# Optimization experiments

Hardware: AMD Instinct MI355X
Metric: run time of the kernel (lower is better)

## Reference

```python
import jax, jax.numpy as jnp
import numpy as np

NX, NY, D, K = 20000, 50000, 64, 8
NUM_BATCHES = 2


def _knn_np(px, py, bx, by, k):
    # Batched exact kNN via chunked squared-distance + argpartition (mirrors torch_cluster.knn under no_grad).
    pp = (px * px).sum(1)
    idx = np.empty((py.shape[0], k), np.int32)
    chunk = 4096
    for s in range(0, py.shape[0], chunk):
        q = py[s:s + chunk]
        d = (q * q).sum(1)[:, None] + pp[None, :] - 2.0 * (q @ px.T)
        d = np.where(by[s:s + chunk, None] == bx[None, :], d, np.inf)
        idx[s:s + chunk] = np.argpartition(d, k, axis=1)[:, :k].astype(np.int32)
    return idx


def setup_inputs() -> dict:
    rng = np.random.default_rng(0)
    pos_x = (rng.random((NX, 3)) * 10.0).astype(np.float32)
    pos_y = (rng.random((NY, 3)) * 10.0).astype(np.float32)
    bx = np.repeat(np.arange(NUM_BATCHES), NX // NUM_BATCHES).astype(np.int32)
    by = np.repeat(np.arange(NUM_BATCHES), NY // NUM_BATCHES).astype(np.int32)
    x_idx = _knn_np(pos_x, pos_y, bx, by, K).reshape(-1)            # [NY*K]
    y_idx = np.repeat(np.arange(NY, dtype=np.int32), K)             # [NY*K]

    key = jax.random.key(0)
    ks = jax.random.split(key, 6)

    def lin(k, fi, fo):
        return jax.random.normal(k, (fi, fo), jnp.float32) / np.sqrt(fi).astype(np.float32)

    return {
        "x": jax.random.normal(ks[0], (NX, D), jnp.float32),
        "pos_x": jnp.asarray(pos_x),
        "pos_y": jnp.asarray(pos_y),
        "x_idx": jnp.asarray(x_idx),
        "y_idx": jnp.asarray(y_idx),
        # ResnetBlockFC 1: size_in=D+3, size_h=D, size_out=D (shortcut linear, no bias)
        "W0a": lin(ks[1], D + 3, D), "b0a": jnp.zeros((D,), jnp.float32),
        "W1a": lin(ks[2], D, D),     "b1a": jnp.zeros((D,), jnp.float32),
        "Wsa": lin(ks[3], D + 3, D),
        # ResnetBlockFC 2: size_in=size_h=size_out=D (identity shortcut)
        "W0b": lin(ks[4], D, D),     "b0b": jnp.zeros((D,), jnp.float32),
        "W1b": lin(ks[5], D, D),     "b1b": jnp.zeros((D,), jnp.float32),
    }


def reference(x, pos_x, pos_y, x_idx, y_idx, W0a, b0a, W1a, b1a, Wsa, W0b, b0b, W1b, b1b):
    # gather + positional diff (diff computed under no_grad in the original)
    diff = jax.lax.stop_gradient(pos_x[x_idx] - pos_y[y_idx])        # [E, 3]
    h = jnp.concatenate([x[x_idx], diff], axis=1)                    # [E, D+3]
    # ResnetBlockFC 1: out = shortcut(h) + fc1(relu(fc0(relu(h))))
    net = jax.nn.relu(h) @ W0a + b0a
    dx = jax.nn.relu(net) @ W1a + b1a
    h = h @ Wsa + dx                                                 # [E, D]
    # ResnetBlockFC 2 (identity shortcut)
    net = jax.nn.relu(h) @ W0b + b0b
    h = h + jax.nn.relu(net) @ W1b + b1b                             # [E, D]
    # scatter-max back to query points (every query has exactly K edges)
    out = jax.ops.segment_max(h, y_idx, num_segments=NY)             # [NY, D]
    return out
```

## Files before the change

kernel.cpp:

```cpp
#include <hip/hip_runtime.h>


typedef _Float16 f16x8 __attribute__((ext_vector_type(8)));
typedef float    f32x4 __attribute__((ext_vector_type(4)));

constexpr int NROWS   = 50000 * 8;
constexpr int NTILES  = NROWS / 16;
constexpr int NFRAG   = 48;
constexpr int TSTRIDE = 72;
constexpr int BW      = 8;

__global__ __launch_bounds__(512, 4)
void pointnet_fused(const float* __restrict__ x,
                    const float* __restrict__ pos_x,
                    const float* __restrict__ pos_y,
                    const int*   __restrict__ x_idx,
                    const float* __restrict__ W0a, const float* __restrict__ b0a,
                    const float* __restrict__ W1a, const float* __restrict__ b1a,
                    const float* __restrict__ Wsa,
                    const float* __restrict__ W0b, const float* __restrict__ b0b,
                    const float* __restrict__ W1b, const float* __restrict__ b1b,
                    float* __restrict__ out)
{
    __shared__ __align__(16) _Float16 bfrag[NFRAG * 64 * 8];
    __shared__ __align__(16) _Float16 trans[BW][16 * TSTRIDE];

    const int tid = threadIdx.x;

    for (int p = tid; p < NFRAG * 64; p += 512) {
        const int f = p >> 6;
        const int l = p & 63;
        const float* W; int krows, fl;
        if (f < 12)      { W = W0a; krows = 67; fl = f; }
        else if (f < 20) { W = W1a; krows = 64; fl = f - 12; }
        else if (f < 32) { W = Wsa; krows = 67; fl = f - 20; }
        else if (f < 40) { W = W0b; krows = 64; fl = f - 32; }
        else             { W = W1b; krows = 64; fl = f - 40; }
        const int s = fl >> 2, t = fl & 3;
        const int n = t * 16 + (l & 15);
        const int kbase = s * 32 + (l >> 4) * 8;
        f16x8 v;
#pragma unroll
        for (int j = 0; j < 8; ++j) {
            const int k = kbase + j;
            v[j] = (_Float16)((k < krows) ? W[k * 64 + n] : 0.0f);
        }
        *(f16x8*)&bfrag[p * 8] = v;
    }
    __syncthreads();

    const int lane = tid & 63;
    const int wv   = tid >> 6;
    const int n0   = lane & 15;
    const int q    = lane >> 4;

    float bias0a[4], bias1a[4], bias0b[4], bias1b[4];
#pragma unroll
    for (int t = 0; t < 4; ++t) {
        bias0a[t] = b0a[t * 16 + n0];
        bias1a[t] = b1a[t * 16 + n0];
        bias0b[t] = b0b[t * 16 + n0];
        bias1b[t] = b1b[t * 16 + n0];
    }

    _Float16* tbuf = trans[wv];
    const int gwave  = blockIdx.x * BW + wv;
    const int nwaves = gridDim.x * BW;

    for (int tile = gwave; tile < NTILES; tile += nwaves) {
        const int row = tile * 16 + n0;
        const int xi  = x_idx[row];
        const float* xp = x + (long)xi * 64;
        f16x8 hn[3], hr[3];
#pragma unroll
        for (int s = 0; s < 2; ++s) {
            const float4* src = (const float4*)(xp + s * 32 + q * 8);
            float4 v0 = src[0], v1 = src[1];
            float vals[8] = {v0.x, v0.y, v0.z, v0.w, v1.x, v1.y, v1.z, v1.w};
#pragma unroll
            for (int j = 0; j < 8; ++j) {
                const float fv = vals[j];
                hn[s][j] = (_Float16)fv;
                hr[s][j] = (_Float16)(fv > 0.0f ? fv : 0.0f);
            }
        }
        {
            f16x8 z = {};
            hn[2] = z; hr[2] = z;
            if (q == 0) {
                const int yi = row >> 3;
#pragma unroll
                for (int j = 0; j < 3; ++j) {
                    const float d = pos_x[xi * 3 + j] - pos_y[yi * 3 + j];
                    hn[2][j] = (_Float16)d;
                    hr[2][j] = (_Float16)(d > 0.0f ? d : 0.0f);
                }
            }
        }

        f32x4 acc[4];
#pragma unroll
        for (int t = 0; t < 4; ++t)
            acc[t] = (f32x4){bias0a[t], bias0a[t], bias0a[t], bias0a[t]};
#pragma unroll
        for (int s = 0; s < 3; ++s)
#pragma unroll
            for (int t = 0; t < 4; ++t) {
                f16x8 b = *(const f16x8*)&bfrag[((s * 4 + t) * 64 + lane) * 8];
                acc[t] = __builtin_amdgcn_mfma_f32_16x16x32_f16(hr[s], b, acc[t], 0, 0, 0);
            }

        __threadfence_block();
#pragma unroll
        for (int t = 0; t < 4; ++t)
#pragma unroll
            for (int r = 0; r < 4; ++r) {
                float v = acc[t][r];
                tbuf[(q * 4 + r) * TSTRIDE + t * 16 + n0] = (_Float16)(v > 0.0f ? v : 0.0f);
            }
        __threadfence_block();
        f16x8 a2[2];
#pragma unroll
        for (int s = 0; s < 2; ++s)
            a2[s] = *(const f16x8*)&tbuf[n0 * TSTRIDE + s * 32 + q * 8];

        f32x4 acc2[4];
#pragma unroll
        for (int t = 0; t < 4; ++t)
            acc2[t] = (f32x4){bias1a[t], bias1a[t], bias1a[t], bias1a[t]};
#pragma unroll
        for (int s = 0; s < 2; ++s)
#pragma unroll
            for (int t = 0; t < 4; ++t) {
                f16x8 b = *(const f16x8*)&bfrag[((12 + s * 4 + t) * 64 + lane) * 8];
                acc2[t] = __builtin_amdgcn_mfma_f32_16x16x32_f16(a2[s], b, acc2[t], 0, 0, 0);
            }
#pragma unroll
        for (int s = 0; s < 3; ++s)
#pragma unroll
            for (int t = 0; t < 4; ++t) {
                f16x8 b = *(const f16x8*)&bfrag[((20 + s * 4 + t) * 64 + lane) * 8];
                acc2[t] = __builtin_amdgcn_mfma_f32_16x16x32_f16(hn[s], b, acc2[t], 0, 0, 0);
            }

        __threadfence_block();
#pragma unroll
        for (int t = 0; t < 4; ++t)
#pragma unroll
            for (int r = 0; r < 4; ++r) {
                float v = acc2[t][r];
                tbuf[(q * 4 + r) * TSTRIDE + t * 16 + n0] = (_Float16)(v > 0.0f ? v : 0.0f);
            }
        __threadfence_block();
        f16x8 a4[2];
#pragma unroll
        for (int s = 0; s < 2; ++s)
            a4[s] = *(const f16x8*)&tbuf[n0 * TSTRIDE + s * 32 + q * 8];

        f32x4 acc3[4];
#pragma unroll
        for (int t = 0; t < 4; ++t)
            acc3[t] = (f32x4){bias0b[t], bias0b[t], bias0b[t], bias0b[t]};
#pragma unroll
        for (int s = 0; s < 2; ++s)
#pragma unroll
            for (int t = 0; t < 4; ++t) {
                f16x8 b = *(const f16x8*)&bfrag[((32 + s * 4 + t) * 64 + lane) * 8];
                acc3[t] = __builtin_amdgcn_mfma_f32_16x16x32_f16(a4[s], b, acc3[t], 0, 0, 0);
            }

        __threadfence_block();
#pragma unroll
        for (int t = 0; t < 4; ++t)
#pragma unroll
            for (int r = 0; r < 4; ++r) {
                float v = acc3[t][r];
                tbuf[(q * 4 + r) * TSTRIDE + t * 16 + n0] = (_Float16)(v > 0.0f ? v : 0.0f);
            }
        __threadfence_block();
        f16x8 a5[2];
#pragma unroll
        for (int s = 0; s < 2; ++s)
            a5[s] = *(const f16x8*)&tbuf[n0 * TSTRIDE + s * 32 + q * 8];

        f32x4 acc4[4];
#pragma unroll
        for (int t = 0; t < 4; ++t) {
            acc4[t] = acc2[t];
            acc4[t][0] += bias1b[t]; acc4[t][1] += bias1b[t];
            acc4[t][2] += bias1b[t]; acc4[t][3] += bias1b[t];
        }
#pragma unroll
        for (int s = 0; s < 2; ++s)
#pragma unroll
            for (int t = 0; t < 4; ++t) {
                f16x8 b = *(const f16x8*)&bfrag[((40 + s * 4 + t) * 64 + lane) * 8];
                acc4[t] = __builtin_amdgcn_mfma_f32_16x16x32_f16(a5[s], b, acc4[t], 0, 0, 0);
            }

#pragma unroll
        for (int t = 0; t < 4; ++t) {
            float pm = fmaxf(fmaxf(acc4[t][0], acc4[t][1]),
                             fmaxf(acc4[t][2], acc4[t][3]));
            pm = fmaxf(pm, __shfl_xor(pm, 16, 64));
            if ((q & 1) == 0) {
                const int y = tile * 2 + (q >> 1);
                out[(long)y * 64 + t * 16 + n0] = pm;
            }
        }
    }
}

extern "C" void kernel_launch(void* const* d_in, const int* in_sizes, int n_in,
                              void* d_out, int out_size, void* d_ws, size_t ws_size,
                              hipStream_t stream) {
    (void)in_sizes; (void)n_in; (void)d_ws; (void)ws_size; (void)out_size;
    pointnet_fused<<<512, 512, 0, stream>>>(
        (const float*)d_in[0],
        (const float*)d_in[1],
        (const float*)d_in[2],
        (const int*)  d_in[3],
        (const float*)d_in[5],  (const float*)d_in[6],
        (const float*)d_in[7],  (const float*)d_in[8],
        (const float*)d_in[9],
        (const float*)d_in[10], (const float*)d_in[11],
        (const float*)d_in[12], (const float*)d_in[13],
        (float*)d_out);
}
```

Measured before the change: 126.6 us.

## Process two 16-row tiles per wave with interleaved MFMAs and atomic work queue

Each wave now handles a pair of 16-row tiles at once, interleaving the two tiles' MFMA chains so independent matrix ops can hide each other's latency, and sharing each B-fragment LDS load across both tiles. Static grid-stride tile assignment is replaced by a global atomic counter (reset with a memset in the workspace) that hands out tile pairs dynamically for load balancing. This raises register pressure, which could cut occupancy or cause spills under the 512x4 launch bound, and adds one atomic per pair plus a memset launch.

```diff
diff --git a/kernel.cpp b/kernel.cpp
--- a/kernel.cpp
+++ b/kernel.cpp
@@ -5,10 +5,36 @@
 typedef float    f32x4 __attribute__((ext_vector_type(4)));
 
 constexpr int NROWS   = 50000 * 8;
-constexpr int NTILES  = NROWS / 16;
+constexpr int NPAIRS  = NROWS / 32;
 constexpr int NFRAG   = 48;
 constexpr int TSTRIDE = 72;
 constexpr int BW      = 8;
+
+static __device__ __forceinline__ f16x8 relu8(f16x8 v) {
+    f16x8 r;
+#pragma unroll
+    for (int j = 0; j < 8; ++j) {
+        _Float16 x = v[j];
+        r[j] = x > (_Float16)0 ? x : (_Float16)0;
+    }
+    return r;
+}
+
+static __device__ __forceinline__ void xpose_relu(const f32x4* acc, _Float16* tbuf,
+                                                  int q, int n0, f16x8* af) {
+    __threadfence_block();
+#pragma unroll
+    for (int t = 0; t < 4; ++t)
+#pragma unroll
+        for (int r = 0; r < 4; ++r) {
+            float v = acc[t][r];
+            tbuf[(q * 4 + r) * TSTRIDE + t * 16 + n0] = (_Float16)(v > 0.0f ? v : 0.0f);
+        }
+    __threadfence_block();
+#pragma unroll
+    for (int s = 0; s < 2; ++s)
+        af[s] = *(const f16x8*)&tbuf[n0 * TSTRIDE + s * 32 + q * 8];
+}
 
 __global__ __launch_bounds__(512, 4)
 void pointnet_fused(const float* __restrict__ x,
@@ -20,7 +46,8 @@
                     const float* __restrict__ Wsa,
                     const float* __restrict__ W0b, const float* __restrict__ b0b,
                     const float* __restrict__ W1b, const float* __restrict__ b1b,
-                    float* __restrict__ out)
+                    float* __restrict__ out,
+                    int* __restrict__ ctr)
 {
     __shared__ __align__(16) _Float16 bfrag[NFRAG * 64 * 8];
     __shared__ __align__(16) _Float16 trans[BW][16 * TSTRIDE];
@@ -64,157 +91,148 @@
     }
 
     _Float16* tbuf = trans[wv];
-    const int gwave  = blockIdx.x * BW + wv;
-    const int nwaves = gridDim.x * BW;
-
-    for (int tile = gwave; tile < NTILES; tile += nwaves) {
-        const int row = tile * 16 + n0;
-        const int xi  = x_idx[row];
-        const float* xp = x + (long)xi * 64;
-        f16x8 hn[3], hr[3];
-#pragma unroll
-        for (int s = 0; s < 2; ++s) {
-            const float4* src = (const float4*)(xp + s * 32 + q * 8);
-            float4 v0 = src[0], v1 = src[1];
-            float vals[8] = {v0.x, v0.y, v0.z, v0.w, v1.x, v1.y, v1.z, v1.w};
-#pragma unroll
-            for (int j = 0; j < 8; ++j) {
-                const float fv = vals[j];
-                hn[s][j] = (_Float16)fv;
-                hr[s][j] = (_Float16)(fv > 0.0f ? fv : 0.0f);
-            }
-        }
-        {
+
+    for (;;) {
+        int pr = 0;
+        if (lane == 0) pr = atomicAdd(ctr, 1);
+        pr = __shfl(pr, 0, 64);
+        if (pr >= NPAIRS) break;
+
+        f16x8 hn[2][3];
+#pragma unroll
+        for (int u = 0; u < 2; ++u) {
+            const int row = pr * 32 + u * 16 + n0;
+            const int xi  = x_idx[row];
+            const float* xp = x + (long)xi * 64;
+#pragma unroll
+            for (int s = 0; s < 2; ++s) {
+                const float4* src = (const float4*)(xp + s * 32 + q * 8);
+                float4 v0 = src[0], v1 = src[1];
+                float vals[8] = {v0.x, v0.y, v0.z, v0.w, v1.x, v1.y, v1.z, v1.w};
+#pragma unroll
+                for (int j = 0; j < 8; ++j)
+                    hn[u][s][j] = (_Float16)vals[j];
+            }
             f16x8 z = {};
-            hn[2] = z; hr[2] = z;
+            hn[u][2] = z;
             if (q == 0) {
                 const int yi = row >> 3;
 #pragma unroll
-                for (int j = 0; j < 3; ++j) {
-                    const float d = pos_x[xi * 3 + j] - pos_y[yi * 3 + j];
-                    hn[2][j] = (_Float16)d;
-                    hr[2][j] = (_Float16)(d > 0.0f ? d : 0.0f);
+                for (int j = 0; j < 3; ++j)
+                    hn[u][2][j] = (_Float16)(pos_x[xi * 3 + j] - pos_y[yi * 3 + j]);
+            }
+        }
+
+        f16x8 hr[2][3];
+#pragma unroll
+        for (int u = 0; u < 2; ++u)
+#pragma unroll
+            for (int s = 0; s < 3; ++s)
+                hr[u][s] = relu8(hn[u][s]);
+
+        f32x4 A1[2][4];
+#pragma unroll
+        for (int u = 0; u < 2; ++u)
+#pragma unroll
+            for (int t = 0; t < 4; ++t)
+                A1[u][t] = (f32x4){bias0a[t], bias0a[t], bias0a[t], bias0a[t]};
+#pragma unroll
+        for (int s = 0; s < 3; ++s)
+#pragma unroll
+            for (int t = 0; t < 4; ++t) {
+                f16x8 b = *(const f16x8*)&bfrag[((s * 4 + t) * 64 + lane) * 8];
+                A1[0][t] = __builtin_amdgcn_mfma_f32_16x16x32_f16(hr[0][s], b, A1[0][t], 0, 0, 0);
+                A1[1][t] = __builtin_amdgcn_mfma_f32_16x16x32_f16(hr[1][s], b, A1[1][t], 0, 0, 0);
+            }
+
+        f16x8 a2[2][2];
+        xpose_relu(A1[0], tbuf, q, n0, a2[0]);
+        xpose_relu(A1[1], tbuf, q, n0, a2[1]);
+
+        f32x4 A2[2][4];
+#pragma unroll
+        for (int u = 0; u < 2; ++u)
+#pragma unroll
+            for (int t = 0; t < 4; ++t)
+                A2[u][t] = (f32x4){bias1a[t], bias1a[t], bias1a[t], bias1a[t]};
+#pragma unroll
+        for (int s = 0; s < 2; ++s)
+#pragma unroll
+            for (int t = 0; t < 4; ++t) {
+                f16x8 b = *(const f16x8*)&bfrag[((12 + s * 4 + t) * 64 + lane) * 8];
+                A2[0][t] = __builtin_amdgcn_mfma_f32_16x16x32_f16(a2[0][s], b, A2[0][t], 0, 0, 0);
+                A2[1][t] = __builtin_amdgcn_mfma_f32_16x16x32_f16(a2[1][s], b, A2[1][t], 0, 0, 0);
+            }
+#pragma unroll
+        for (int s = 0; s < 3; ++s)
+#pragma unroll
+            for (int t = 0; t < 4; ++t) {
+                f16x8 b = *(const f16x8*)&bfrag[((20 + s * 4 + t) * 64 + lane) * 8];
+                A2[0][t] = __builtin_amdgcn_mfma_f32_16x16x32_f16(hn[0][s], b, A2[0][t], 0, 0, 0);
+                A2[1][t] = __builtin_amdgcn_mfma_f32_16x16x32_f16(hn[1][s], b, A2[1][t], 0, 0, 0);
+            }
+
+        f16x8 a4[2][2];
+        xpose_relu(A2[0], tbuf, q, n0, a4[0]);
+        xpose_relu(A2[1], tbuf, q, n0, a4[1]);
+
+        f32x4 A3[2][4];
+#pragma unroll
+        for (int u = 0; u < 2; ++u)
+#pragma unroll
+            for (int t = 0; t < 4; ++t)
+                A3[u][t] = (f32x4){bias0b[t], bias0b[t], bias0b[t], bias0b[t]};
+#pragma unroll
+        for (int s = 0; s < 2; ++s)
+#pragma unroll
+            for (int t = 0; t < 4; ++t) {
+                f16x8 b = *(const f16x8*)&bfrag[((32 + s * 4 + t) * 64 + lane) * 8];
+                A3[0][t] = __builtin_amdgcn_mfma_f32_16x16x32_f16(a4[0][s], b, A3[0][t], 0, 0, 0);
+                A3[1][t] = __builtin_amdgcn_mfma_f32_16x16x32_f16(a4[1][s], b, A3[1][t], 0, 0, 0);
+            }
+
+        f16x8 a5[2][2];
+        xpose_relu(A3[0], tbuf, q, n0, a5[0]);
+        xpose_relu(A3[1], tbuf, q, n0, a5[1]);
+
+        f32x4 A4[2][4];
+#pragma unroll
+        for (int u = 0; u < 2; ++u)
+#pragma unroll
+            for (int t = 0; t < 4; ++t) {
+                A4[u][t] = A2[u][t];
+                A4[u][t][0] += bias1b[t]; A4[u][t][1] += bias1b[t];
+                A4[u][t][2] += bias1b[t]; A4[u][t][3] += bias1b[t];
+            }
+#pragma unroll
+        for (int s = 0; s < 2; ++s)
+#pragma unroll
+            for (int t = 0; t < 4; ++t) {
+                f16x8 b = *(const f16x8*)&bfrag[((40 + s * 4 + t) * 64 + lane) * 8];
+                A4[0][t] = __builtin_amdgcn_mfma_f32_16x16x32_f16(a5[0][s], b, A4[0][t], 0, 0, 0);
+                A4[1][t] = __builtin_amdgcn_mfma_f32_16x16x32_f16(a5[1][s], b, A4[1][t], 0, 0, 0);
+            }
+
+#pragma unroll
+        for (int u = 0; u < 2; ++u)
+#pragma unroll
+            for (int t = 0; t < 4; ++t) {
+                float pm = fmaxf(fmaxf(A4[u][t][0], A4[u][t][1]),
+                                 fmaxf(A4[u][t][2], A4[u][t][3]));
+                pm = fmaxf(pm, __shfl_xor(pm, 16, 64));
+                if ((q & 1) == 0) {
+                    const int y = pr * 4 + u * 2 + (q >> 1);
+                    out[(long)y * 64 + t * 16 + n0] = pm;
                 }
             }
-        }
-
-        f32x4 acc[4];
-#pragma unroll
-        for (int t = 0; t < 4; ++t)
-            acc[t] = (f32x4){bias0a[t], bias0a[t], bias0a[t], bias0a[t]};
-#pragma unroll
-        for (int s = 0; s < 3; ++s)
-#pragma unroll
-            for (int t = 0; t < 4; ++t) {
-                f16x8 b = *(const f16x8*)&bfrag[((s * 4 + t) * 64 + lane) * 8];
-                acc[t] = __builtin_amdgcn_mfma_f32_16x16x32_f16(hr[s], b, acc[t], 0, 0, 0);
-            }
-
-        __threadfence_block();
-#pragma unroll
-        for (int t = 0; t < 4; ++t)
-#pragma unroll
-            for (int r = 0; r < 4; ++r) {
-                float v = acc[t][r];
-                tbuf[(q * 4 + r) * TSTRIDE + t * 16 + n0] = (_Float16)(v > 0.0f ? v : 0.0f);
-            }
-        __threadfence_block();
-        f16x8 a2[2];
-#pragma unroll
-        for (int s = 0; s < 2; ++s)
-            a2[s] = *(const f16x8*)&tbuf[n0 * TSTRIDE + s * 32 + q * 8];
-
-        f32x4 acc2[4];
-#pragma unroll
-        for (int t = 0; t < 4; ++t)
-            acc2[t] = (f32x4){bias1a[t], bias1a[t], bias1a[t], bias1a[t]};
-#pragma unroll
-        for (int s = 0; s < 2; ++s)
-#pragma unroll
-            for (int t = 0; t < 4; ++t) {
-                f16x8 b = *(const f16x8*)&bfrag[((12 + s * 4 + t) * 64 + lane) * 8];
-                acc2[t] = __builtin_amdgcn_mfma_f32_16x16x32_f16(a2[s], b, acc2[t], 0, 0, 0);
-            }
-#pragma unroll
-        for (int s = 0; s < 3; ++s)
-#pragma unroll
-            for (int t = 0; t < 4; ++t) {
-                f16x8 b = *(const f16x8*)&bfrag[((20 + s * 4 + t) * 64 + lane) * 8];
-                acc2[t] = __builtin_amdgcn_mfma_f32_16x16x32_f16(hn[s], b, acc2[t], 0, 0, 0);
-            }
-
-        __threadfence_block();
-#pragma unroll
-        for (int t = 0; t < 4; ++t)
-#pragma unroll
-            for (int r = 0; r < 4; ++r) {
-                float v = acc2[t][r];
-                tbuf[(q * 4 + r) * TSTRIDE + t * 16 + n0] = (_Float16)(v > 0.0f ? v : 0.0f);
-            }
-        __threadfence_block();
-        f16x8 a4[2];
-#pragma unroll
-        for (int s = 0; s < 2; ++s)
-            a4[s] = *(const f16x8*)&tbuf[n0 * TSTRIDE + s * 32 + q * 8];
-
-        f32x4 acc3[4];
-#pragma unroll
-        for (int t = 0; t < 4; ++t)
-            acc3[t] = (f32x4){bias0b[t], bias0b[t], bias0b[t], bias0b[t]};
-#pragma unroll
-        for (int s = 0; s < 2; ++s)
-#pragma unroll
-            for (int t = 0; t < 4; ++t) {
-                f16x8 b = *(const f16x8*)&bfrag[((32 + s * 4 + t) * 64 + lane) * 8];
-                acc3[t] = __builtin_amdgcn_mfma_f32_16x16x32_f16(a4[s], b, acc3[t], 0, 0, 0);
-            }
-
-        __threadfence_block();
-#pragma unroll
-        for (int t = 0; t < 4; ++t)
-#pragma unroll
-            for (int r = 0; r < 4; ++r) {
-                float v = acc3[t][r];
-                tbuf[(q * 4 + r) * TSTRIDE + t * 16 + n0] = (_Float16)(v > 0.0f ? v : 0.0f);
-            }
-        __threadfence_block();
-        f16x8 a5[2];
-#pragma unroll
-        for (int s = 0; s < 2; ++s)
-            a5[s] = *(const f16x8*)&tbuf[n0 * TSTRIDE + s * 32 + q * 8];
-
-        f32x4 acc4[4];
-#pragma unroll
-        for (int t = 0; t < 4; ++t) {
-            acc4[t] = acc2[t];
-            acc4[t][0] += bias1b[t]; acc4[t][1] += bias1b[t];
-            acc4[t][2] += bias1b[t]; acc4[t][3] += bias1b[t];
-        }
-#pragma unroll
-        for (int s = 0; s < 2; ++s)
-#pragma unroll
-            for (int t = 0; t < 4; ++t) {
-                f16x8 b = *(const f16x8*)&bfrag[((40 + s * 4 + t) * 64 + lane) * 8];
-                acc4[t] = __builtin_amdgcn_mfma_f32_16x16x32_f16(a5[s], b, acc4[t], 0, 0, 0);
-            }
-
-#pragma unroll
-        for (int t = 0; t < 4; ++t) {
-            float pm = fmaxf(fmaxf(acc4[t][0], acc4[t][1]),
-                             fmaxf(acc4[t][2], acc4[t][3]));
-            pm = fmaxf(pm, __shfl_xor(pm, 16, 64));
-            if ((q & 1) == 0) {
-                const int y = tile * 2 + (q >> 1);
-                out[(long)y * 64 + t * 16 + n0] = pm;
-            }
-        }
     }
 }
 
 extern "C" void kernel_launch(void* const* d_in, const int* in_sizes, int n_in,
                               void* d_out, int out_size, void* d_ws, size_t ws_size,
                               hipStream_t stream) {
-    (void)in_sizes; (void)n_in; (void)d_ws; (void)ws_size; (void)out_size;
+    (void)in_sizes; (void)n_in; (void)ws_size; (void)out_size;
+    hipMemsetAsync(d_ws, 0, 64, stream);
     pointnet_fused<<<512, 512, 0, stream>>>(
         (const float*)d_in[0],
         (const float*)d_in[1],
@@ -225,5 +243,6 @@
         (const float*)d_in[9],
         (const float*)d_in[10], (const float*)d_in[11],
         (const float*)d_in[12], (const float*)d_in[13],
-        (float*)d_out);
-}
+        (float*)d_out,
+        (int*)d_ws);
+}
```

Measured after the change: 291.3 us. +130.1%, slower.
